# Kernel tuning notes

Hardware: AMD Instinct MI355X
Metric: run time of the kernel (lower is better)

The kernel has to match this reference:

```python
import jax, jax.numpy as jnp
import numpy as np

B, S, H = 2, 2048, 1024
E, I = 8, 4096
TOP_K = 2
W_SCALE = 0.02


def setup_inputs() -> dict:
    key = jax.random.key(0)
    k1, k2, k3, k4, k5 = jax.random.split(key, 5)
    return {
        "hidden_states": jax.random.normal(k1, (B, S, H), dtype=jnp.float32),
        "gate_w": jax.random.normal(k2, (H, E), dtype=jnp.float32) * W_SCALE,
        "w1s": jax.random.normal(k3, (E, H, I), dtype=jnp.float32) * W_SCALE,
        "w2s": jax.random.normal(k4, (E, I, H), dtype=jnp.float32) * W_SCALE,
        "w3s": jax.random.normal(k5, (E, H, I), dtype=jnp.float32) * W_SCALE,
    }


def reference(hidden_states, gate_w, w1s, w2s, w3s):
    b, s, h = hidden_states.shape
    x = hidden_states.reshape(-1, h)                      # [T, H]
    # Router: softmax in fp32, top-k, renormalize (matches torch F.softmax(dtype=float) + topk)
    logits = x @ gate_w                                   # [T, E]
    probs = jax.nn.softmax(logits.astype(jnp.float32), axis=-1)
    rw, sel = jax.lax.top_k(probs, TOP_K)                 # [T, K], [T, K]
    rw = rw / jnp.sum(rw, axis=-1, keepdims=True)
    # Per-token combine weight for each expert: [T, E]
    comb = jnp.sum(jax.nn.one_hot(sel, E, dtype=x.dtype) * rw[..., None].astype(x.dtype), axis=1)
    # Expert SwiGLU MLPs; loop over small fixed expert count (same math as grouped GEMM + scatter)
    out = jnp.zeros_like(x)
    for e in range(E):
        inter = jax.nn.silu(x @ w1s[e]) * (x @ w3s[e])    # [T, I]
        out = out + comb[:, e:e + 1] * (inter @ w2s[e])   # [T, H]
    return out.reshape(b, s, h)
```

## Files before the change

### kernel.cpp

```cpp
#include <hip/hip_runtime.h>

#define T_TOK 4096
#define H_DIM 1024
#define I_DIM 4096
#define NE 8
#define INTER_ROWS 9216

typedef _Float16 f16;
typedef _Float16 f16x8 __attribute__((ext_vector_type(8)));
typedef _Float16 f16x4 __attribute__((ext_vector_type(4)));
typedef float f32x4 __attribute__((ext_vector_type(4)));

#define GLOBAL_AS __attribute__((address_space(1)))
#define LDS_AS __attribute__((address_space(3)))

__device__ __forceinline__ void gload_lds16(const void* g, void* l) {
  __builtin_amdgcn_global_load_lds((GLOBAL_AS const unsigned int*)g,
                                   (LDS_AS unsigned int*)l, 16, 0, 0);
}

#define VM0() asm volatile("s_waitcnt vmcnt(0)" ::: "memory")
#define BARF()                          \
  do {                                  \
    asm volatile("" ::: "memory");      \
    __builtin_amdgcn_s_barrier();       \
    asm volatile("" ::: "memory");      \
  } while (0)
#define PRIO1() __builtin_amdgcn_s_setprio(1)
#define PRIO0() __builtin_amdgcn_s_setprio(0)

__global__ void cast_x_kernel(const float* __restrict__ x, f16* __restrict__ xh) {
  int i = blockIdx.x * 256 + threadIdx.x;
  float4 v = reinterpret_cast<const float4*>(x)[i];
  f16x4 o = {(f16)v.x, (f16)v.y, (f16)v.z, (f16)v.w};
  reinterpret_cast<f16x4*>(xh)[i] = o;
}

__global__ __launch_bounds__(256) void transpose_cast_kernel(
    const float* __restrict__ w1s, const float* __restrict__ w3s,
    const float* __restrict__ w2s, f16* __restrict__ w13t, f16* __restrict__ w2t) {
  __shared__ float tile[64][65];
  const int z = blockIdx.z;
  const int tr = threadIdx.x >> 4;
  const int tc = (threadIdx.x & 15) * 4;
  if (z < 16) {
    int e = z & 7;
    const float* in = (z < 8 ? w1s : w3s) + (size_t)e * H_DIM * I_DIM;
    f16* out = w13t + (size_t)e * (2 * H_DIM * I_DIM);
    const int roff = (z < 8) ? 0 : 32;
    const int c0 = blockIdx.x * 64, r0 = blockIdx.y * 64;
#pragma unroll
    for (int i = 0; i < 4; ++i) {
      int r = tr + i * 16;
      float4 v = *reinterpret_cast<const float4*>(&in[(size_t)(r0 + r) * I_DIM + c0 + tc]);
      tile[r][tc] = v.x; tile[r][tc + 1] = v.y; tile[r][tc + 2] = v.z; tile[r][tc + 3] = v.w;
    }
    __syncthreads();
#pragma unroll
    for (int i = 0; i < 4; ++i) {
      int oc = tr + i * 16;
      int cg = c0 + oc;
      int rowo = ((cg >> 5) << 6) + roff + (cg & 31);
      f16x4 h;
#pragma unroll
      for (int j = 0; j < 4; ++j) h[j] = (f16)tile[tc + j][oc];
      *reinterpret_cast<f16x4*>(&out[(size_t)rowo * H_DIM + r0 + tc]) = h;
    }
  } else {
    int e = z - 16;
    const float* in = w2s + (size_t)e * H_DIM * I_DIM;
    f16* out = w2t + (size_t)e * H_DIM * I_DIM;
    const int r0 = blockIdx.x * 64, c0 = blockIdx.y * 64;
#pragma unroll
    for (int i = 0; i < 4; ++i) {
      int r = tr + i * 16;
      float4 v = *reinterpret_cast<const float4*>(&in[(size_t)(r0 + r) * H_DIM + c0 + tc]);
      tile[r][tc] = v.x; tile[r][tc + 1] = v.y; tile[r][tc + 2] = v.z; tile[r][tc + 3] = v.w;
    }
    __syncthreads();
#pragma unroll
    for (int i = 0; i < 4; ++i) {
      int oc = tr + i * 16;
      f16x4 h;
#pragma unroll
      for (int j = 0; j < 4; ++j) h[j] = (f16)tile[tc + j][oc];
      *reinterpret_cast<f16x4*>(&out[(size_t)(c0 + oc) * I_DIM + r0 + tc]) = h;
    }
  }
}

__global__ void router_kernel(const float* __restrict__ x, const float* __restrict__ gw,
                              int* __restrict__ counts, int* __restrict__ lists,
                              float* __restrict__ wgts) {
  const int t = blockIdx.x;
  const int l = threadIdx.x;
  const float* xr = x + (size_t)t * H_DIM;
  float acc[NE];
#pragma unroll
  for (int e = 0; e < NE; ++e) acc[e] = 0.f;
  for (int k = l; k < H_DIM; k += 64) {
    float xv = xr[k];
#pragma unroll
    for (int e = 0; e < NE; ++e) acc[e] += xv * gw[k * NE + e];
  }
#pragma unroll
  for (int e = 0; e < NE; ++e) {
    float v = acc[e];
#pragma unroll
    for (int off = 32; off > 0; off >>= 1) v += __shfl_xor(v, off);
    acc[e] = v;
  }
  if (l == 0) {
    int i1 = 0;
#pragma unroll
    for (int e = 1; e < NE; ++e)
      if (acc[e] > acc[i1]) i1 = e;
    int i2 = (i1 == 0) ? 1 : 0;
#pragma unroll
    for (int e = 0; e < NE; ++e)
      if (e != i1 && acc[e] > acc[i2]) i2 = e;
    float wA = 1.f / (1.f + __expf(acc[i2] - acc[i1]));
    float wB = 1.f - wA;
    int p1 = atomicAdd(&counts[i1], 1);
    lists[i1 * T_TOK + p1] = t;
    wgts[i1 * T_TOK + p1] = wA;
    int p2 = atomicAdd(&counts[i2], 1);
    lists[i2 * T_TOK + p2] = t;
    wgts[i2 * T_TOK + p2] = wB;
  }
}

__global__ void prefix_kernel(const int* __restrict__ counts, int* __restrict__ bases) {
  if (threadIdx.x == 0) {
    int s = 0;
#pragma unroll
    for (int e = 0; e < NE; ++e) {
      bases[e] = s;
      s += (counts[e] + 127) & ~127;
    }
  }
}

__global__ __launch_bounds__(512, 1) void gemm_a_kernel(
    const f16* __restrict__ xh, const f16* __restrict__ w13t,
    const int* __restrict__ counts, const int* __restrict__ bases,
    const int* __restrict__ lists, f16* __restrict__ inter) {
  const int z = blockIdx.z;
  const int cnt = counts[z];
  const int r0 = blockIdx.y * 256;
  if (r0 >= cnt) return;
  const int base = bases[z], pad = (cnt + 127) & ~127;
  const int c0 = blockIdx.x * 256;
  const int tid = threadIdx.x, lane = tid & 63, wid = tid >> 6;
  const int wm = wid >> 2, wn = wid & 3, lrow = lane & 15, lk = lane >> 4;

  __shared__ __align__(16) f16 lds[2][32768];

  const int* lst = lists + z * T_TOK;
  const f16* w13 = w13t + (size_t)z * (2 * H_DIM * I_DIM);

  const f16* sp[4][2];
  f16* dp[4][2];
#pragma unroll
  for (int j = 0; j < 2; ++j) {
    int cg = (wid * 2 + j) * 64 + lane;
    int rih = cg >> 3;
    int loct = (cg & 7) ^ (rih & 7);
    int t0 = lst[r0 + rih], t1 = lst[r0 + 128 + rih];
    sp[0][j] = xh + (size_t)t0 * H_DIM + loct * 8;
    sp[2][j] = xh + (size_t)t1 * H_DIM + loct * 8;
    sp[1][j] = w13 + (size_t)(c0 + rih) * H_DIM + loct * 8;
    sp[3][j] = w13 + (size_t)(c0 + 128 + rih) * H_DIM + loct * 8;
    dp[0][j] = &lds[0][cg * 8];
    dp[2][j] = &lds[0][8192 + cg * 8];
    dp[1][j] = &lds[0][16384 + cg * 8];
    dp[3][j] = &lds[0][24576 + cg * 8];
  }

#define STG(u, S, K)                                        \
  do {                                                      \
    gload_lds16(sp[u][0] + (K), dp[u][0] + (S) * 32768);    \
    gload_lds16(sp[u][1] + (K), dp[u][1] + (S) * 32768);    \
  } while (0)

#define LDA(kh)                                                                        \
  {                                                                                    \
    _Pragma("unroll") for (int m_ = 0; m_ < 8; ++m_) {                                 \
      int row = wm * 128 + m_ * 16 + lrow;                                             \
      af[m_] = *reinterpret_cast<const f16x8*>(                                        \
          &SA[row * 64 + (((kh) * 4 + lk) ^ (row & 7)) * 8]);                          \
    }                                                                                  \
  }
#define LDB(kh, np)                                                                    \
  {                                                                                    \
    _Pragma("unroll") for (int n_ = 0; n_ < 2; ++n_) {                                 \
      int row = wn * 64 + ((np) * 2 + n_) * 16 + lrow;                                 \
      bf[n_] = *reinterpret_cast<const f16x8*>(                                        \
          &SB[row * 64 + (((kh) * 4 + lk) ^ (row & 7)) * 8]);                          \
    }                                                                                  \
  }
#define MF(np)                                                                         \
  {                                                                                    \
    PRIO1();                                                                           \
    _Pragma("unroll") for (int m_ = 0; m_ < 8; ++m_)                                   \
        _Pragma("unroll") for (int n_ = 0; n_ < 2; ++n_)                               \
            acc[m_][(np) * 2 + n_] = __builtin_amdgcn_mfma_f32_16x16x32_f16(           \
                af[m_], bf[n_], acc[m_][(np) * 2 + n_], 0, 0, 0);                      \
    PRIO0();                                                                           \
  }

  const f32x4 z4 = {0.f, 0.f, 0.f, 0.f};
  f32x4 acc[8][4];
#pragma unroll
  for (int m = 0; m < 8; ++m)
#pragma unroll
    for (int n = 0; n < 4; ++n) acc[m][n] = z4;

  const int NT = H_DIM / 64;
  STG(0, 0, 0); STG(1, 0, 0); STG(2, 0, 0); STG(3, 0, 0);

  for (int t = 0; t < NT; ++t) {
    const f16* SA = lds[t & 1];
    const f16* SB = SA + 16384;
    const int S = (t + 1) & 1;
    const int ks = (t + 1 < NT ? t + 1 : NT - 1) * 64;
    f16x8 af[8], bf[2];
    VM0();
    BARF();
    STG(0, S, ks); STG(1, S, ks);
    LDA(0); LDB(0, 0); MF(0);
    BARF();
    STG(2, S, ks); STG(3, S, ks);
    LDB(0, 1); MF(1);
    BARF();
    LDA(1); LDB(1, 0); MF(0);
    BARF();
    LDB(1, 1); MF(1);
  }
#undef STG
#undef LDA
#undef LDB
#undef MF

#pragma unroll
  for (int m = 0; m < 8; ++m)
#pragma unroll
    for (int r = 0; r < 4; ++r) {
      int rowl = wm * 128 + m * 16 + lk * 4 + r;
      if (r0 + rowl < pad) {
        size_t grow = base + r0 + rowl;
#pragma unroll
        for (int n = 0; n < 2; ++n) {
          int col = (c0 >> 1) + wn * 32 + n * 16 + lrow;
          float v1 = acc[m][n][r];
          float v3 = acc[m][n + 2][r];
          float sv = v1 / (1.f + __expf(-v1));
          inter[grow * I_DIM + col] = (f16)(sv * v3);
        }
      }
    }
}

__global__ __launch_bounds__(512, 1) void gemm_b_kernel(
    const f16* __restrict__ inter, const f16* __restrict__ w2t,
    const int* __restrict__ counts, const int* __restrict__ bases,
    const int* __restrict__ lists, const float* __restrict__ wgts,
    float* __restrict__ out) {
  const int z = blockIdx.z;
  const int cnt = counts[z];
  const int rb = blockIdx.y >> 1, kb = blockIdx.y & 1;
  const int r0 = rb * 256;
  if (r0 >= cnt) return;
  const int base = bases[z];
  const int c0 = blockIdx.x * 256;
  const int tid = threadIdx.x, lane = tid & 63, wid = tid >> 6;
  const int wm = wid >> 2, wn = wid & 3, lrow = lane & 15, lk = lane >> 4;

  __shared__ __align__(16) f16 lds[2][32768];

  const int* lst = lists + z * T_TOK;
  const float* wgt = wgts + z * T_TOK;
  const f16* w2 = w2t + (size_t)z * I_DIM * H_DIM;
  const int K0 = kb * 2048;

  const f16* sp[4][2];
  f16* dp[4][2];
#pragma unroll
  for (int j = 0; j < 2; ++j) {
    int cg = (wid * 2 + j) * 64 + lane;
    int rih = cg >> 3;
    int loct = (cg & 7) ^ (rih & 7);
    sp[0][j] = inter + (size_t)(base + r0 + rih) * I_DIM + K0 + loct * 8;
    sp[2][j] = inter + (size_t)(base + r0 + 128 + rih) * I_DIM + K0 + loct * 8;
    sp[1][j] = w2 + (size_t)(c0 + rih) * I_DIM + K0 + loct * 8;
    sp[3][j] = w2 + (size_t)(c0 + 128 + rih) * I_DIM + K0 + loct * 8;
    dp[0][j] = &lds[0][cg * 8];
    dp[2][j] = &lds[0][8192 + cg * 8];
    dp[1][j] = &lds[0][16384 + cg * 8];
    dp[3][j] = &lds[0][24576 + cg * 8];
  }

#define STG(u, S, K)                                        \
  do {                                                      \
    gload_lds16(sp[u][0] + (K), dp[u][0] + (S) * 32768);    \
    gload_lds16(sp[u][1] + (K), dp[u][1] + (S) * 32768);    \
  } while (0)

#define LDA(kh)                                                                        \
  {                                                                                    \
    _Pragma("unroll") for (int m_ = 0; m_ < 8; ++m_) {                                 \
      int row = wm * 128 + m_ * 16 + lrow;                                             \
      af[m_] = *reinterpret_cast<const f16x8*>(                                        \
          &SA[row * 64 + (((kh) * 4 + lk) ^ (row & 7)) * 8]);                          \
    }                                                                                  \
  }
#define LDB(kh, np)                                                                    \
  {                                                                                    \
    _Pragma("unroll") for (int n_ = 0; n_ < 2; ++n_) {                                 \
      int row = wn * 64 + ((np) * 2 + n_) * 16 + lrow;                                 \
      bf[n_] = *reinterpret_cast<const f16x8*>(                                        \
          &SB[row * 64 + (((kh) * 4 + lk) ^ (row & 7)) * 8]);                          \
    }                                                                                  \
  }
#define MF(np)                                                                         \
  {                                                                                    \
    PRIO1();                                                                           \
    _Pragma("unroll") for (int m_ = 0; m_ < 8; ++m_)                                   \
        _Pragma("unroll") for (int n_ = 0; n_ < 2; ++n_)                               \
            acc[m_][(np) * 2 + n_] = __builtin_amdgcn_mfma_f32_16x16x32_f16(           \
                af[m_], bf[n_], acc[m_][(np) * 2 + n_], 0, 0, 0);                      \
    PRIO0();                                                                           \
  }

  const f32x4 z4 = {0.f, 0.f, 0.f, 0.f};
  f32x4 acc[8][4];
#pragma unroll
  for (int m = 0; m < 8; ++m)
#pragma unroll
    for (int n = 0; n < 4; ++n) acc[m][n] = z4;

  const int NT = 2048 / 64;
  STG(0, 0, 0); STG(1, 0, 0); STG(2, 0, 0); STG(3, 0, 0);

  for (int t = 0; t < NT; ++t) {
    const f16* SA = lds[t & 1];
    const f16* SB = SA + 16384;
    const int S = (t + 1) & 1;
    const int ks = (t + 1 < NT ? t + 1 : NT - 1) * 64;
    f16x8 af[8], bf[2];
    VM0();
    BARF();
    STG(0, S, ks); STG(1, S, ks);
    LDA(0); LDB(0, 0); MF(0);
    BARF();
    STG(2, S, ks); STG(3, S, ks);
    LDB(0, 1); MF(1);
    BARF();
    LDA(1); LDB(1, 0); MF(0);
    BARF();
    LDB(1, 1); MF(1);
  }
#undef STG
#undef LDA
#undef LDB
#undef MF

#pragma unroll
  for (int m = 0; m < 8; ++m)
#pragma unroll
    for (int r = 0; r < 4; ++r) {
      int ri = r0 + wm * 128 + m * 16 + lk * 4 + r;
      if (ri < cnt) {
        int tok = lst[ri];
        float wg = wgt[ri];
        float* orow = out + (size_t)tok * H_DIM + c0 + wn * 64 + lrow;
#pragma unroll
        for (int n = 0; n < 4; ++n) atomicAdd(&orow[n * 16], wg * acc[m][n][r]);
      }
    }
}

extern "C" void kernel_launch(void* const* d_in, const int* in_sizes, int n_in,
                              void* d_out, int out_size, void* d_ws, size_t ws_size,
                              hipStream_t stream) {
  const float* x = (const float*)d_in[0];
  const float* gw = (const float*)d_in[1];
  const float* w1s = (const float*)d_in[2];
  const float* w2s = (const float*)d_in[3];
  const float* w3s = (const float*)d_in[4];
  float* out = (float*)d_out;

  char* ws = (char*)d_ws;
  f16* xh = (f16*)ws;
  f16* inter = (f16*)(ws + ((size_t)8 << 20));
  f16* w13t = (f16*)(ws + ((size_t)80 << 20));
  f16* w2t = (f16*)(ws + ((size_t)208 << 20));
  char* meta = ws + ((size_t)272 << 20);
  int* counts = (int*)meta;
  int* bases = (int*)(meta + 512);
  int* lists = (int*)(meta + 1024);
  float* wgts = (float*)(meta + 1024 + (size_t)NE * T_TOK * 4);

  hipMemsetAsync(out, 0, (size_t)out_size * sizeof(float), stream);
  hipMemsetAsync(meta, 0, 1024 + (size_t)NE * T_TOK * 8, stream);

  cast_x_kernel<<<dim3((T_TOK * H_DIM) / (4 * 256)), dim3(256), 0, stream>>>(x, xh);
  router_kernel<<<dim3(T_TOK), dim3(64), 0, stream>>>(x, gw, counts, lists, wgts);
  prefix_kernel<<<dim3(1), dim3(64), 0, stream>>>(counts, bases);
  transpose_cast_kernel<<<dim3(64, 16, 24), dim3(256), 0, stream>>>(
      w1s, w3s, w2s, w13t, w2t);
  gemm_a_kernel<<<dim3((2 * I_DIM) / 256, T_TOK / 256, NE), dim3(512), 0, stream>>>(
      xh, w13t, counts, bases, lists, inter);
  gemm_b_kernel<<<dim3(H_DIM / 256, 2 * (T_TOK / 256), NE), dim3(512), 0, stream>>>(
      inter, w2t, counts, bases, lists, wgts, out);
}
```

Baseline: 549.1 us.

## Software-pipeline MFMA fragment loads, remap blocks across XCDs, widen transpose stores

Both expert GEMM kernels now load LDS fragments into double-buffered registers, so the next k-step's A/B fragments are read while the current MFMAs run. Redundant loads on the last iteration are skipped. The grids are flattened and block indices remapped so blocks sharing weight columns land on the same XCD, aiming for better L2 reuse. The transpose-cast kernel writes 16-byte f16x8 stores instead of 8-byte ones. The register-prefetch buffers raise VGPR pressure and may cause spills.

```diff
diff --git a/kernel.cpp b/kernel.cpp
--- a/kernel.cpp
+++ b/kernel.cpp
@@ -57,14 +57,16 @@
     }
     __syncthreads();
 #pragma unroll
-    for (int i = 0; i < 4; ++i) {
-      int oc = tr + i * 16;
+    for (int it = 0; it < 2; ++it) {
+      int idx = it * 256 + threadIdx.x;
+      int oc = idx >> 3;
+      int ch = (idx & 7) * 8;
       int cg = c0 + oc;
       int rowo = ((cg >> 5) << 6) + roff + (cg & 31);
-      f16x4 h;
-#pragma unroll
-      for (int j = 0; j < 4; ++j) h[j] = (f16)tile[tc + j][oc];
-      *reinterpret_cast<f16x4*>(&out[(size_t)rowo * H_DIM + r0 + tc]) = h;
+      f16x8 h;
+#pragma unroll
+      for (int j = 0; j < 8; ++j) h[j] = (f16)tile[ch + j][oc];
+      *reinterpret_cast<f16x8*>(&out[(size_t)rowo * H_DIM + r0 + ch]) = h;
     }
   } else {
     int e = z - 16;
@@ -79,12 +81,14 @@
     }
     __syncthreads();
 #pragma unroll
-    for (int i = 0; i < 4; ++i) {
-      int oc = tr + i * 16;
-      f16x4 h;
-#pragma unroll
-      for (int j = 0; j < 4; ++j) h[j] = (f16)tile[tc + j][oc];
-      *reinterpret_cast<f16x4*>(&out[(size_t)(c0 + oc) * I_DIM + r0 + tc]) = h;
+    for (int it = 0; it < 2; ++it) {
+      int idx = it * 256 + threadIdx.x;
+      int oc = idx >> 3;
+      int ch = (idx & 7) * 8;
+      f16x8 h;
+#pragma unroll
+      for (int j = 0; j < 8; ++j) h[j] = (f16)tile[ch + j][oc];
+      *reinterpret_cast<f16x8*>(&out[(size_t)(c0 + oc) * I_DIM + r0 + ch]) = h;
     }
   }
 }
@@ -141,16 +145,46 @@
   }
 }
 
+#define LDAm(DST, kh, SBASE)                                                      \
+  {                                                                               \
+    _Pragma("unroll") for (int m_ = 0; m_ < 8; ++m_) {                            \
+      int row = wm * 128 + m_ * 16 + lrow;                                        \
+      DST[m_] = *reinterpret_cast<const f16x8*>(                                  \
+          &SBASE[row * 64 + (((kh)*4 + lk) ^ (row & 7)) * 8]);                    \
+    }                                                                             \
+  }
+#define LDBm(DST, kh, np, SBBASE)                                                 \
+  {                                                                               \
+    _Pragma("unroll") for (int n_ = 0; n_ < 2; ++n_) {                            \
+      int row = wn * 64 + ((np)*2 + n_) * 16 + lrow;                              \
+      DST[n_] = *reinterpret_cast<const f16x8*>(                                  \
+          &SBBASE[row * 64 + (((kh)*4 + lk) ^ (row & 7)) * 8]);                   \
+    }                                                                             \
+  }
+#define MFm(AF, BF, np)                                                           \
+  {                                                                               \
+    PRIO1();                                                                      \
+    _Pragma("unroll") for (int m_ = 0; m_ < 8; ++m_)                              \
+        _Pragma("unroll") for (int n_ = 0; n_ < 2; ++n_)                          \
+            acc[m_][(np)*2 + n_] = __builtin_amdgcn_mfma_f32_16x16x32_f16(        \
+                AF[m_], BF[n_], acc[m_][(np)*2 + n_], 0, 0, 0);                   \
+    PRIO0();                                                                      \
+  }
+
 __global__ __launch_bounds__(512, 1) void gemm_a_kernel(
     const f16* __restrict__ xh, const f16* __restrict__ w13t,
     const int* __restrict__ counts, const int* __restrict__ bases,
     const int* __restrict__ lists, f16* __restrict__ inter) {
+  const int w = blockIdx.x;
+  const int xcd = w & 7, q = w >> 3;
+  const int bx = xcd * 4 + (q & 3);
+  const int by = q >> 2;
   const int z = blockIdx.z;
   const int cnt = counts[z];
-  const int r0 = blockIdx.y * 256;
+  const int r0 = by * 256;
   if (r0 >= cnt) return;
   const int base = bases[z], pad = (cnt + 127) & ~127;
-  const int c0 = blockIdx.x * 256;
+  const int c0 = bx * 256;
   const int tid = threadIdx.x, lane = tid & 63, wid = tid >> 6;
   const int wm = wid >> 2, wn = wid & 3, lrow = lane & 15, lk = lane >> 4;
 
@@ -179,35 +213,9 @@
 
 #define STG(u, S, K)                                        \
   do {                                                      \
-    gload_lds16(sp[u][0] + (K), dp[u][0] + (S) * 32768);    \
-    gload_lds16(sp[u][1] + (K), dp[u][1] + (S) * 32768);    \
+    gload_lds16(sp[u][0] + (K), dp[u][0] + (S)*32768);      \
+    gload_lds16(sp[u][1] + (K), dp[u][1] + (S)*32768);      \
   } while (0)
-
-#define LDA(kh)                                                                        \
-  {                                                                                    \
-    _Pragma("unroll") for (int m_ = 0; m_ < 8; ++m_) {                                 \
-      int row = wm * 128 + m_ * 16 + lrow;                                             \
-      af[m_] = *reinterpret_cast<const f16x8*>(                                        \
-          &SA[row * 64 + (((kh) * 4 + lk) ^ (row & 7)) * 8]);                          \
-    }                                                                                  \
-  }
-#define LDB(kh, np)                                                                    \
-  {                                                                                    \
-    _Pragma("unroll") for (int n_ = 0; n_ < 2; ++n_) {                                 \
-      int row = wn * 64 + ((np) * 2 + n_) * 16 + lrow;                                 \
-      bf[n_] = *reinterpret_cast<const f16x8*>(                                        \
-          &SB[row * 64 + (((kh) * 4 + lk) ^ (row & 7)) * 8]);                          \
-    }                                                                                  \
-  }
-#define MF(np)                                                                         \
-  {                                                                                    \
-    PRIO1();                                                                           \
-    _Pragma("unroll") for (int m_ = 0; m_ < 8; ++m_)                                   \
-        _Pragma("unroll") for (int n_ = 0; n_ < 2; ++n_)                               \
-            acc[m_][(np) * 2 + n_] = __builtin_amdgcn_mfma_f32_16x16x32_f16(           \
-                af[m_], bf[n_], acc[m_][(np) * 2 + n_], 0, 0, 0);                      \
-    PRIO0();                                                                           \
-  }
 
   const f32x4 z4 = {0.f, 0.f, 0.f, 0.f};
   f32x4 acc[8][4];
@@ -216,31 +224,40 @@
 #pragma unroll
     for (int n = 0; n < 4; ++n) acc[m][n] = z4;
 
+  f16x8 afA[8], afB[8], bfX[2], bfY[2];
   const int NT = H_DIM / 64;
+
   STG(0, 0, 0); STG(1, 0, 0); STG(2, 0, 0); STG(3, 0, 0);
+  VM0(); BARF();
+  { const f16* SA = lds[0]; const f16* SB = SA + 16384;
+    LDAm(afA, 0, SA); LDBm(bfX, 0, 0, SB); }
 
   for (int t = 0; t < NT; ++t) {
     const f16* SA = lds[t & 1];
     const f16* SB = SA + 16384;
     const int S = (t + 1) & 1;
-    const int ks = (t + 1 < NT ? t + 1 : NT - 1) * 64;
-    f16x8 af[8], bf[2];
+    const f16* SA2 = lds[S];
+    const f16* SB2 = SA2 + 16384;
+    const bool more = (t + 1 < NT);
+    const int ks = (t + 1) * 64;
+    if (more) { STG(0, S, ks); STG(1, S, ks); }
+    LDBm(bfY, 0, 1, SB);
+    BARF();
+    MFm(afA, bfX, 0);
+    if (more) { STG(2, S, ks); STG(3, S, ks); }
+    LDAm(afB, 1, SA);
+    LDBm(bfX, 1, 0, SB);
+    BARF();
+    MFm(afA, bfY, 1);
+    LDBm(bfY, 1, 1, SB);
+    BARF();
+    MFm(afB, bfX, 0);
     VM0();
     BARF();
-    STG(0, S, ks); STG(1, S, ks);
-    LDA(0); LDB(0, 0); MF(0);
-    BARF();
-    STG(2, S, ks); STG(3, S, ks);
-    LDB(0, 1); MF(1);
-    BARF();
-    LDA(1); LDB(1, 0); MF(0);
-    BARF();
-    LDB(1, 1); MF(1);
+    if (more) { LDAm(afA, 0, SA2); LDBm(bfX, 0, 0, SB2); }
+    MFm(afB, bfY, 1);
   }
 #undef STG
-#undef LDA
-#undef LDB
-#undef MF
 
 #pragma unroll
   for (int m = 0; m < 8; ++m)
@@ -266,13 +283,17 @@
     const int* __restrict__ counts, const int* __restrict__ bases,
     const int* __restrict__ lists, const float* __restrict__ wgts,
     float* __restrict__ out) {
+  const int w = blockIdx.x;
+  const int xcd = w & 7, q = w >> 3;
+  const int bx = xcd >> 1;
+  const int yid = (xcd & 1) * 16 + q;
+  const int rb = yid >> 1, kb = yid & 1;
   const int z = blockIdx.z;
   const int cnt = counts[z];
-  const int rb = blockIdx.y >> 1, kb = blockIdx.y & 1;
   const int r0 = rb * 256;
   if (r0 >= cnt) return;
   const int base = bases[z];
-  const int c0 = blockIdx.x * 256;
+  const int c0 = bx * 256;
   const int tid = threadIdx.x, lane = tid & 63, wid = tid >> 6;
   const int wm = wid >> 2, wn = wid & 3, lrow = lane & 15, lk = lane >> 4;
 
@@ -302,35 +323,9 @@
 
 #define STG(u, S, K)                                        \
   do {                                                      \
-    gload_lds16(sp[u][0] + (K), dp[u][0] + (S) * 32768);    \
-    gload_lds16(sp[u][1] + (K), dp[u][1] + (S) * 32768);    \
+    gload_lds16(sp[u][0] + (K), dp[u][0] + (S)*32768);      \
+    gload_lds16(sp[u][1] + (K), dp[u][1] + (S)*32768);      \
   } while (0)
-
-#define LDA(kh)                                                                        \
-  {                                                                                    \
-    _Pragma("unroll") for (int m_ = 0; m_ < 8; ++m_) {                                 \
-      int row = wm * 128 + m_ * 16 + lrow;                                             \
-      af[m_] = *reinterpret_cast<const f16x8*>(                                        \
-          &SA[row * 64 + (((kh) * 4 + lk) ^ (row & 7)) * 8]);                          \
-    }                                                                                  \
-  }
-#define LDB(kh, np)                                                                    \
-  {                                                                                    \
-    _Pragma("unroll") for (int n_ = 0; n_ < 2; ++n_) {                                 \
-      int row = wn * 64 + ((np) * 2 + n_) * 16 + lrow;                                 \
-      bf[n_] = *reinterpret_cast<const f16x8*>(                                        \
-          &SB[row * 64 + (((kh) * 4 + lk) ^ (row & 7)) * 8]);                          \
-    }                                                                                  \
-  }
-#define MF(np)                                                                         \
-  {                                                                                    \
-    PRIO1();                                                                           \
-    _Pragma("unroll") for (int m_ = 0; m_ < 8; ++m_)                                   \
-        _Pragma("unroll") for (int n_ = 0; n_ < 2; ++n_)                               \
-            acc[m_][(np) * 2 + n_] = __builtin_amdgcn_mfma_f32_16x16x32_f16(           \
-                af[m_], bf[n_], acc[m_][(np) * 2 + n_], 0, 0, 0);                      \
-    PRIO0();                                                                           \
-  }
 
   const f32x4 z4 = {0.f, 0.f, 0.f, 0.f};
   f32x4 acc[8][4];
@@ -339,31 +334,40 @@
 #pragma unroll
     for (int n = 0; n < 4; ++n) acc[m][n] = z4;
 
+  f16x8 afA[8], afB[8], bfX[2], bfY[2];
   const int NT = 2048 / 64;
+
   STG(0, 0, 0); STG(1, 0, 0); STG(2, 0, 0); STG(3, 0, 0);
+  VM0(); BARF();
+  { const f16* SA = lds[0]; const f16* SB = SA + 16384;
+    LDAm(afA, 0, SA); LDBm(bfX, 0, 0, SB); }
 
   for (int t = 0; t < NT; ++t) {
     const f16* SA = lds[t & 1];
     const f16* SB = SA + 16384;
     const int S = (t + 1) & 1;
-    const int ks = (t + 1 < NT ? t + 1 : NT - 1) * 64;
-    f16x8 af[8], bf[2];
+    const f16* SA2 = lds[S];
+    const f16* SB2 = SA2 + 16384;
+    const bool more = (t + 1 < NT);
+    const int ks = (t + 1) * 64;
+    if (more) { STG(0, S, ks); STG(1, S, ks); }
+    LDBm(bfY, 0, 1, SB);
+    BARF();
+    MFm(afA, bfX, 0);
+    if (more) { STG(2, S, ks); STG(3, S, ks); }
+    LDAm(afB, 1, SA);
+    LDBm(bfX, 1, 0, SB);
+    BARF();
+    MFm(afA, bfY, 1);
+    LDBm(bfY, 1, 1, SB);
+    BARF();
+    MFm(afB, bfX, 0);
     VM0();
     BARF();
-    STG(0, S, ks); STG(1, S, ks);
-    LDA(0); LDB(0, 0); MF(0);
-    BARF();
-    STG(2, S, ks); STG(3, S, ks);
-    LDB(0, 1); MF(1);
-    BARF();
-    LDA(1); LDB(1, 0); MF(0);
-    BARF();
-    LDB(1, 1); MF(1);
+    if (more) { LDAm(afA, 0, SA2); LDBm(bfX, 0, 0, SB2); }
+    MFm(afB, bfY, 1);
   }
 #undef STG
-#undef LDA
-#undef LDB
-#undef MF
 
 #pragma unroll
   for (int m = 0; m < 8; ++m)
@@ -409,8 +413,8 @@
   prefix_kernel<<<dim3(1), dim3(64), 0, stream>>>(counts, bases);
   transpose_cast_kernel<<<dim3(64, 16, 24), dim3(256), 0, stream>>>(
       w1s, w3s, w2s, w13t, w2t);
-  gemm_a_kernel<<<dim3((2 * I_DIM) / 256, T_TOK / 256, NE), dim3(512), 0, stream>>>(
+  gemm_a_kernel<<<dim3(512, 1, NE), dim3(512), 0, stream>>>(
       xh, w13t, counts, bases, lists, inter);
-  gemm_b_kernel<<<dim3(H_DIM / 256, 2 * (T_TOK / 256), NE), dim3(512), 0, stream>>>(
+  gemm_b_kernel<<<dim3(128, 1, NE), dim3(512), 0, stream>>>(
       inter, w2t, counts, bases, lists, wgts, out);
 }
```

Result: slower. 611.3 us (+11.3%).
